# Kernel optimization log

Measured on AMD Instinct MI355X. Metric: run time of the kernel, lower is better.

The kernel has to match this reference:

```python
import jax, jax.numpy as jnp
import numpy as np

BIGINT = 1e10
BOA, BOH, BOL = 21, 22, 23      # global-node residue symbols
ATOM_POS_PAD = 0                # atom position pad index
AG_SEG = 1                      # antigen segment id


def setup_inputs() -> dict:
    key = jax.random.key(0)
    ks = jax.random.split(key, 8)
    B, L, C, E = 16, 128, 14, 256
    N = B * L
    # residues with global tokens at fixed positions per protein
    S = jax.random.randint(ks[0], (B, L), 0, 21)
    S = S.at[:, 0].set(BOA).at[:, 48].set(BOH).at[:, 96].set(BOL)
    S = S.reshape(N)
    seg = np.zeros((L,), np.int32); seg[0:48] = 1; seg[48:96] = 2; seg[96:] = 3
    segment_ids = jnp.tile(jnp.asarray(seg), B)
    RP = jnp.tile(jnp.arange(L, dtype=jnp.int32), B)
    A = jax.random.randint(ks[1], (N, C), 1, 16)
    AP = jax.random.randint(ks[2], (N, C), 0, 16)
    AP = AP.at[:, :4].set(jnp.arange(1, 5, dtype=AP.dtype)[None, :])  # backbone always present
    X = jax.random.normal(ks[3], (N, C, 3), dtype=jnp.float32) * 3.0
    res_embed = jax.random.normal(ks[4], (25, E), dtype=jnp.float32) * 0.02
    atom_embed = jax.random.normal(ks[5], (16, E), dtype=jnp.float32) * 0.02
    atom_pos_embed = jax.random.normal(ks[6], (16, E), dtype=jnp.float32) * 0.02
    return dict(S=S, RP=RP, A=A, AP=AP, X=X, segment_ids=segment_ids,
                res_embed=res_embed, atom_embed=atom_embed,
                atom_pos_embed=atom_pos_embed, max_n=L, k_neighbors=9)


def _embed(S, RP, A, AP, res_embed, atom_embed, atom_pos_embed):
    N = S.shape[0]
    E = res_embed.shape[1]
    half = E // 2
    inv = jnp.power(10000.0, -2.0 * jnp.arange(half, dtype=jnp.float32) / E)
    ang = RP.astype(jnp.float32)[:, None] * inv[None, :]
    pos_e = jnp.stack([jnp.sin(ang), jnp.cos(ang)], axis=-1).reshape(N, E)
    res_e = res_embed[S] + pos_e
    atom_e = atom_embed[A] + atom_pos_embed[AP]            # [N,C,E]
    not_pad = (AP != ATOM_POS_PAD)
    denom = not_pad.sum(-1, keepdims=True).astype(res_e.dtype) + 1e-10
    atom_e = jnp.sum(atom_e * not_pad[..., None], axis=1) / denom
    return jnp.concatenate([res_e, atom_e], axis=-1)       # [N,2E]


def _min_pair_dist(X, AP, max_n):
    # min over atom pairs of ||X[i,a]-X[j,b]||, pad atoms pushed to BIGINT
    N, C, _ = X.shape
    B = N // max_n
    Xb = X.reshape(B, max_n, C, 3)
    pad = (AP == ATOM_POS_PAD).reshape(B, max_n, C)
    sq = jnp.sum(Xb * Xb, axis=-1)                          # [B,L,C]
    dot = jnp.einsum('biad,bjcd->biajc', Xb, Xb)            # [B,L,C,L,C]
    d2 = sq[:, :, :, None, None] + sq[:, None, None, :, :] - 2.0 * dot
    dist = jnp.sqrt(jnp.maximum(d2, 0.0))
    pmask = pad[:, :, :, None, None] | pad[:, None, None, :, :]
    dist = dist + pmask.astype(dist.dtype) * BIGINT
    return jnp.min(dist, axis=(2, 4))                       # [B,L,L]


def _knn(dist_mat, sel_mask, k):
    # smallest-k neighbors among selected candidate edges; invalid -> -1
    B, L, _ = dist_mat.shape
    d = jnp.where(sel_mask, dist_mat, BIGINT)
    neg, dst_local = jax.lax.top_k(-d, k)                   # [B,L,k]
    valid = ((-neg) < BIGINT).reshape(-1)
    offs = (jnp.arange(B) * L)[:, None, None]
    src = jnp.broadcast_to(jnp.arange(L)[None, :, None] + offs, (B, L, k)).reshape(-1)
    dst = (dst_local + offs).reshape(-1)
    src = jnp.where(valid, src, -1)
    dst = jnp.where(valid, dst, -1)
    return jnp.stack([src, dst]), valid


def reference(S, RP, A, AP, X, segment_ids, res_embed, atom_embed, atom_pos_embed, max_n, k_neighbors):
    N = S.shape[0]
    L = max_n
    B = N // L
    h = _embed(S, RP, A, AP, res_embed, atom_embed, atom_pos_embed)
    dist = _min_pair_dist(X, AP, L)                          # [B,L,L]
    g = ((S == BOA) | (S == BOH) | (S == BOL)).reshape(B, L)
    seg = segment_ids.reshape(B, L)
    not_self = ~jnp.eye(L, dtype=bool)[None]                 # exclude i==j
    gi, gj = g[:, :, None], g[:, None, :]
    not_global = ~(gi | gj)
    same_seg = seg[:, :, None] == seg[:, None, :]
    inner_mask = same_seg & not_global & not_self
    outer_mask = (~same_seg) & not_global & not_self
    ctx_knn, ctx_valid = _knn(dist, inner_mask, k_neighbors)
    inter_knn, inter_valid = _knn(dist, outer_mask, k_neighbors)
    # non-kNN ctx edges (global_normal | global_global | sequential), dense adjacency
    global_normal = same_seg & (gi | gj) & not_self
    global_global = gi & gj & not_self
    idx = jnp.arange(L)
    adj_seq = (jnp.abs(idx[:, None] - idx[None, :]) == 1)[None]
    seq_mask = adj_seq & not_global & (seg[:, :, None] != AG_SEG)
    extra_ctx_adj = global_normal | global_global | seq_mask  # [B,L,L] bool
    return h, ctx_knn, ctx_valid, extra_ctx_adj, inter_knn, inter_valid
```

## Files before the change

kernel.cpp:

```cpp
#include <hip/hip_runtime.h>
#include <math.h>
#include <float.h>
#include <stdint.h>

#define BIGINT_F 1e10f
#define L_TOK 128
#define C_ATOM 14
#define E_DIM 256
#define K_NB 9

__device__ __forceinline__ float sq3(float x, float y, float z) {
    return __fadd_rn(__fadd_rn(__fmul_rn(x, x), __fmul_rn(y, y)), __fmul_rn(z, z));
}

__device__ __forceinline__ uint64_t umin64(uint64_t a, uint64_t b) { return a < b ? a : b; }

__global__ void __launch_bounds__(256)
fused_kernel(const int* __restrict__ S, const int* __restrict__ RP,
             const int* __restrict__ A, const int* __restrict__ AP,
             const float* __restrict__ X, const int* __restrict__ seg,
             const float* __restrict__ res_embed,
             const float* __restrict__ atom_embed,
             const float* __restrict__ atom_pos_embed,
             float* __restrict__ h,
             float* __restrict__ ctx_src, float* __restrict__ ctx_dst, float* __restrict__ ctx_val,
             float* __restrict__ adj_out,
             float* __restrict__ int_src, float* __restrict__ int_dst, float* __restrict__ int_val,
             int N) {
    const int NKNN = N / 4;
    int blk = blockIdx.x;
    int tid = threadIdx.x;

    if (blk < NKNN) {
        int wave = tid >> 6;
        int lane = tid & 63;
        int bi = blk * 4 + wave;
        int b  = bi >> 7;
        int i  = bi & (L_TOK - 1);
        int base_tok = (b << 7);

        __shared__ float sX[C_ATOM * L_TOK];
        __shared__ float sY[C_ATOM * L_TOK];
        __shared__ float sZ[C_ATOM * L_TOK];
        __shared__ float sQ[C_ATOM * L_TOK];

        const float* Xb  = X  + (size_t)base_tok * C_ATOM * 3;
        const int*   APb = AP + base_tok * C_ATOM;
        for (int idx = tid; idx < L_TOK * C_ATOM; idx += 256) {
            int tok = idx / C_ATOM;
            int c   = idx - tok * C_ATOM;
            float x0 = Xb[idx * 3 + 0];
            float x1 = Xb[idx * 3 + 1];
            float x2 = Xb[idx * 3 + 2];
            float q  = (APb[idx] == 0) ? INFINITY : sq3(x0, x1, x2);
            int w = c * L_TOK + (tok ^ (2 * c));
            sX[w] = x0; sY[w] = x1; sZ[w] = x2; sQ[w] = q;
        }
        __syncthreads();

        float xa0[C_ATOM], xa1[C_ATOM], xa2[C_ATOM], sa[C_ATOM];
        #pragma unroll
        for (int a = 0; a < C_ATOM; ++a) {
            int w = a * L_TOK + (i ^ (2 * a));
            xa0[a] = sX[w]; xa1[a] = sY[w]; xa2[a] = sZ[w]; sa[a] = sQ[w];
        }

        int j0 = lane, j1 = lane + 64;
        int nj0 = base_tok + j0, nj1 = base_tok + j1;

        float mind0 = INFINITY, mind1 = INFINITY;
        for (int c = 0; c < C_ATOM; ++c) {
            int w = c * L_TOK + (lane ^ (2 * c));
            float y00 = sX[w],      y01 = sY[w],      y02 = sZ[w],      sc0 = sQ[w];
            float y10 = sX[w + 64], y11 = sY[w + 64], y12 = sZ[w + 64], sc1 = sQ[w + 64];
            #pragma unroll
            for (int a = 0; a < C_ATOM; ++a) {
                float dot0 = __fadd_rn(__fadd_rn(__fmul_rn(xa0[a], y00),
                                                 __fmul_rn(xa1[a], y01)),
                                       __fmul_rn(xa2[a], y02));
                float d20 = __fsub_rn(__fadd_rn(sa[a], sc0), __fmul_rn(2.0f, dot0));
                mind0 = fminf(mind0, d20);
                float dot1 = __fadd_rn(__fadd_rn(__fmul_rn(xa0[a], y10),
                                                 __fmul_rn(xa1[a], y11)),
                                       __fmul_rn(xa2[a], y12));
                float d21 = __fsub_rn(__fadd_rn(sa[a], sc1), __fmul_rn(2.0f, dot1));
                mind1 = fminf(mind1, d21);
            }
        }
        float d0 = sqrtf(fmaxf(mind0, 0.0f));
        float d1 = sqrtf(fmaxf(mind1, 0.0f));

        int si = S[bi];
        int segi = seg[bi];
        bool gi = si >= 21;
        int sj0 = S[nj0], sj1 = S[nj1];
        int segj0 = seg[nj0], segj1 = seg[nj1];
        bool gj0 = sj0 >= 21, gj1 = sj1 >= 21;
        bool ns0 = (j0 != i), ns1 = (j1 != i);
        bool ng0 = !gi && !gj0 && ns0;
        bool ng1 = !gi && !gj1 && ns1;
        bool inner0 = (segi == segj0) && ng0;
        bool inner1 = (segi == segj1) && ng1;
        bool outer0 = (segi != segj0) && ng0;
        bool outer1 = (segi != segj1) && ng1;

        {
            bool gij0 = gi || gj0, gij1 = gi || gj1;
            bool same0 = (segi == segj0), same1 = (segi == segj1);
            int dd0 = i - j0, dd1 = i - j1;
            bool a0 = (dd0 == 1 || dd0 == -1), a1 = (dd1 == 1 || dd1 == -1);
            bool v0 = (same0 && gij0 && ns0) || (gi && gj0 && ns0) || (a0 && !gij0 && (segi != 1));
            bool v1 = (same1 && gij1 && ns1) || (gi && gj1 && ns1) || (a1 && !gij1 && (segi != 1));
            adj_out[(size_t)bi * L_TOK + j0] = v0 ? 1.0f : 0.0f;
            adj_out[(size_t)bi * L_TOK + j1] = v1 ? 1.0f : 0.0f;
        }

        const uint32_t bigbits = __float_as_uint(BIGINT_F);
        uint64_t kd0 = ((uint64_t)__float_as_uint(d0) << 32) | (uint32_t)j0;
        uint64_t kd1 = ((uint64_t)__float_as_uint(d1) << 32) | (uint32_t)j1;
        uint64_t kbig0 = ((uint64_t)bigbits << 32) | (uint32_t)j0;
        uint64_t kbig1 = ((uint64_t)bigbits << 32) | (uint32_t)j1;

        for (int pass = 0; pass < 2; ++pass) {
            uint64_t k0 = (pass == 0 ? inner0 : outer0) ? kd0 : kbig0;
            uint64_t k1 = (pass == 0 ? inner1 : outer1) ? kd1 : kbig1;
            float* osrc = (pass == 0) ? ctx_src : int_src;
            float* odst = (pass == 0) ? ctx_dst : int_dst;
            float* oval = (pass == 0) ? ctx_val : int_val;
            #pragma unroll
            for (int k = 0; k < K_NB; ++k) {
                uint64_t kk = umin64(k0, k1);
                #pragma unroll
                for (int m = 32; m > 0; m >>= 1) {
                    uint64_t o = __shfl_xor((unsigned long long)kk, m, 64);
                    kk = umin64(kk, o);
                }
                if (k0 == kk) k0 = UINT64_MAX;
                if (k1 == kk) k1 = UINT64_MAX;
                if (lane == 0) {
                    uint32_t dbits = (uint32_t)(kk >> 32);
                    int jmin = (int)(uint32_t)kk;
                    bool valid = dbits < bigbits;
                    int o = bi * K_NB + k;
                    osrc[o] = valid ? (float)bi : -1.0f;
                    odst[o] = valid ? (float)(base_tok + jmin) : -1.0f;
                    oval[o] = valid ? 1.0f : 0.0f;
                }
            }
        }
    } else {
        int n = blk - NKNN;
        int e = tid;
        int s = S[n];
        float rp = (float)RP[n];

        int k = e >> 1;
        const float c1 = (float)(-2.0 * 13.287712379549449 / (double)E_DIM);
        float invk = exp2f((float)k * c1);
        float ang = rp * invk;
        float pe = (e & 1) ? cosf(ang) : sinf(ang);
        h[(size_t)n * (2 * E_DIM) + e] = res_embed[s * E_DIM + e] + pe;

        __shared__ int sA[C_ATOM], sAP[C_ATOM];
        if (e < C_ATOM) { sA[e] = A[n * C_ATOM + e]; sAP[e] = AP[n * C_ATOM + e]; }
        __syncthreads();

        float sum = 0.0f, cnt = 0.0f;
        for (int c = 0; c < C_ATOM; ++c) {
            if (sAP[c] != 0) {
                sum += atom_embed[sA[c] * E_DIM + e] + atom_pos_embed[sAP[c] * E_DIM + e];
                cnt += 1.0f;
            }
        }
        h[(size_t)n * (2 * E_DIM) + E_DIM + e] = sum / (cnt + 1e-10f);
    }
}

extern "C" void kernel_launch(void* const* d_in, const int* in_sizes, int n_in,
                              void* d_out, int out_size, void* d_ws, size_t ws_size,
                              hipStream_t stream) {
    const int*   S    = (const int*)d_in[0];
    const int*   RP   = (const int*)d_in[1];
    const int*   A    = (const int*)d_in[2];
    const int*   AP   = (const int*)d_in[3];
    const float* X    = (const float*)d_in[4];
    const int*   seg  = (const int*)d_in[5];
    const float* rese = (const float*)d_in[6];
    const float* atme = (const float*)d_in[7];
    const float* atpe = (const float*)d_in[8];

    const int N = in_sizes[0];
    const int B = N / L_TOK;
    float* out = (float*)d_out;

    size_t off = 0;
    float* h_out   = out + off;  off += (size_t)N * 2 * E_DIM;
    float* ctx_src = out + off;  off += (size_t)N * K_NB;
    float* ctx_dst = out + off;  off += (size_t)N * K_NB;
    float* ctx_val = out + off;  off += (size_t)N * K_NB;
    float* adj_out = out + off;  off += (size_t)B * L_TOK * L_TOK;
    float* int_src = out + off;  off += (size_t)N * K_NB;
    float* int_dst = out + off;  off += (size_t)N * K_NB;
    float* int_val = out + off;  off += (size_t)N * K_NB;

    int nknn = N / 4;
    int grid = nknn + N;
    fused_kernel<<<grid, 256, 0, stream>>>(S, RP, A, AP, X, seg, rese, atme, atpe,
                                           h_out, ctx_src, ctx_dst, ctx_val,
                                           adj_out, int_src, int_dst, int_val, N);
}
```

Baseline: 97.91 us.

## Fold embedding work into kNN waves with float4 loads and drop separate embed blocks

Removes the N separate embedding blocks and has each kNN wave also compute its token's embedding row. Each lane handles four features using float4 loads and stores of the embedding tables. The launch_bounds hint also requests two blocks per CU. This shrinks the grid and cuts block launch and scheduling overhead, but makes each kNN block longer and its register use higher.

```diff
diff --git a/kernel.cpp b/kernel.cpp
--- a/kernel.cpp
+++ b/kernel.cpp
@@ -15,7 +15,7 @@
 
 __device__ __forceinline__ uint64_t umin64(uint64_t a, uint64_t b) { return a < b ? a : b; }
 
-__global__ void __launch_bounds__(256)
+__global__ void __launch_bounds__(256, 2)
 fused_kernel(const int* __restrict__ S, const int* __restrict__ RP,
              const int* __restrict__ A, const int* __restrict__ AP,
              const float* __restrict__ X, const int* __restrict__ seg,
@@ -27,152 +27,164 @@
              float* __restrict__ adj_out,
              float* __restrict__ int_src, float* __restrict__ int_dst, float* __restrict__ int_val,
              int N) {
-    const int NKNN = N / 4;
     int blk = blockIdx.x;
     int tid = threadIdx.x;
-
-    if (blk < NKNN) {
-        int wave = tid >> 6;
-        int lane = tid & 63;
-        int bi = blk * 4 + wave;
-        int b  = bi >> 7;
-        int i  = bi & (L_TOK - 1);
-        int base_tok = (b << 7);
-
-        __shared__ float sX[C_ATOM * L_TOK];
-        __shared__ float sY[C_ATOM * L_TOK];
-        __shared__ float sZ[C_ATOM * L_TOK];
-        __shared__ float sQ[C_ATOM * L_TOK];
-
-        const float* Xb  = X  + (size_t)base_tok * C_ATOM * 3;
-        const int*   APb = AP + base_tok * C_ATOM;
-        for (int idx = tid; idx < L_TOK * C_ATOM; idx += 256) {
-            int tok = idx / C_ATOM;
-            int c   = idx - tok * C_ATOM;
-            float x0 = Xb[idx * 3 + 0];
-            float x1 = Xb[idx * 3 + 1];
-            float x2 = Xb[idx * 3 + 2];
-            float q  = (APb[idx] == 0) ? INFINITY : sq3(x0, x1, x2);
-            int w = c * L_TOK + (tok ^ (2 * c));
-            sX[w] = x0; sY[w] = x1; sZ[w] = x2; sQ[w] = q;
-        }
-        __syncthreads();
-
-        float xa0[C_ATOM], xa1[C_ATOM], xa2[C_ATOM], sa[C_ATOM];
+    int wave = tid >> 6;
+    int lane = tid & 63;
+    int bi = blk * 4 + wave;
+    int b  = bi >> 7;
+    int i  = bi & (L_TOK - 1);
+    int base_tok = (b << 7);
+
+    __shared__ float sX[C_ATOM * L_TOK];
+    __shared__ float sY[C_ATOM * L_TOK];
+    __shared__ float sZ[C_ATOM * L_TOK];
+    __shared__ float sQ[C_ATOM * L_TOK];
+
+    const float* Xb  = X  + (size_t)base_tok * C_ATOM * 3;
+    const int*   APb = AP + base_tok * C_ATOM;
+    for (int idx = tid; idx < L_TOK * C_ATOM; idx += 256) {
+        int tok = idx / C_ATOM;
+        int c   = idx - tok * C_ATOM;
+        float x0 = Xb[idx * 3 + 0];
+        float x1 = Xb[idx * 3 + 1];
+        float x2 = Xb[idx * 3 + 2];
+        float q  = (APb[idx] == 0) ? INFINITY : sq3(x0, x1, x2);
+        int w = c * L_TOK + (tok ^ (2 * c));
+        sX[w] = x0; sY[w] = x1; sZ[w] = x2; sQ[w] = q;
+    }
+    __syncthreads();
+
+    float xa0[C_ATOM], xa1[C_ATOM], xa2[C_ATOM], sa[C_ATOM];
+    #pragma unroll
+    for (int a = 0; a < C_ATOM; ++a) {
+        int w = a * L_TOK + (i ^ (2 * a));
+        xa0[a] = sX[w]; xa1[a] = sY[w]; xa2[a] = sZ[w]; sa[a] = sQ[w];
+    }
+
+    int j0 = lane, j1 = lane + 64;
+    int nj0 = base_tok + j0, nj1 = base_tok + j1;
+
+    float mind0 = INFINITY, mind1 = INFINITY;
+    for (int c = 0; c < C_ATOM; ++c) {
+        int w = c * L_TOK + (lane ^ (2 * c));
+        float y00 = sX[w],      y01 = sY[w],      y02 = sZ[w],      sc0 = sQ[w];
+        float y10 = sX[w + 64], y11 = sY[w + 64], y12 = sZ[w + 64], sc1 = sQ[w + 64];
         #pragma unroll
         for (int a = 0; a < C_ATOM; ++a) {
-            int w = a * L_TOK + (i ^ (2 * a));
-            xa0[a] = sX[w]; xa1[a] = sY[w]; xa2[a] = sZ[w]; sa[a] = sQ[w];
+            float dot0 = __fadd_rn(__fadd_rn(__fmul_rn(xa0[a], y00),
+                                             __fmul_rn(xa1[a], y01)),
+                                   __fmul_rn(xa2[a], y02));
+            float d20 = __fsub_rn(__fadd_rn(sa[a], sc0), __fmul_rn(2.0f, dot0));
+            mind0 = fminf(mind0, d20);
+            float dot1 = __fadd_rn(__fadd_rn(__fmul_rn(xa0[a], y10),
+                                             __fmul_rn(xa1[a], y11)),
+                                   __fmul_rn(xa2[a], y12));
+            float d21 = __fsub_rn(__fadd_rn(sa[a], sc1), __fmul_rn(2.0f, dot1));
+            mind1 = fminf(mind1, d21);
         }
-
-        int j0 = lane, j1 = lane + 64;
-        int nj0 = base_tok + j0, nj1 = base_tok + j1;
-
-        float mind0 = INFINITY, mind1 = INFINITY;
-        for (int c = 0; c < C_ATOM; ++c) {
-            int w = c * L_TOK + (lane ^ (2 * c));
-            float y00 = sX[w],      y01 = sY[w],      y02 = sZ[w],      sc0 = sQ[w];
-            float y10 = sX[w + 64], y11 = sY[w + 64], y12 = sZ[w + 64], sc1 = sQ[w + 64];
+    }
+    float d0 = sqrtf(fmaxf(mind0, 0.0f));
+    float d1 = sqrtf(fmaxf(mind1, 0.0f));
+
+    int si = S[bi];
+    int segi = seg[bi];
+    bool gi = si >= 21;
+    int sj0 = S[nj0], sj1 = S[nj1];
+    int segj0 = seg[nj0], segj1 = seg[nj1];
+    bool gj0 = sj0 >= 21, gj1 = sj1 >= 21;
+    bool ns0 = (j0 != i), ns1 = (j1 != i);
+    bool ng0 = !gi && !gj0 && ns0;
+    bool ng1 = !gi && !gj1 && ns1;
+    bool inner0 = (segi == segj0) && ng0;
+    bool inner1 = (segi == segj1) && ng1;
+    bool outer0 = (segi != segj0) && ng0;
+    bool outer1 = (segi != segj1) && ng1;
+
+    {
+        bool gij0 = gi || gj0, gij1 = gi || gj1;
+        bool same0 = (segi == segj0), same1 = (segi == segj1);
+        int dd0 = i - j0, dd1 = i - j1;
+        bool a0 = (dd0 == 1 || dd0 == -1), a1 = (dd1 == 1 || dd1 == -1);
+        bool v0 = (same0 && gij0 && ns0) || (gi && gj0 && ns0) || (a0 && !gij0 && (segi != 1));
+        bool v1 = (same1 && gij1 && ns1) || (gi && gj1 && ns1) || (a1 && !gij1 && (segi != 1));
+        adj_out[(size_t)bi * L_TOK + j0] = v0 ? 1.0f : 0.0f;
+        adj_out[(size_t)bi * L_TOK + j1] = v1 ? 1.0f : 0.0f;
+    }
+
+    const uint32_t bigbits = __float_as_uint(BIGINT_F);
+    uint64_t kd0 = ((uint64_t)__float_as_uint(d0) << 32) | (uint32_t)j0;
+    uint64_t kd1 = ((uint64_t)__float_as_uint(d1) << 32) | (uint32_t)j1;
+    uint64_t kbig0 = ((uint64_t)bigbits << 32) | (uint32_t)j0;
+    uint64_t kbig1 = ((uint64_t)bigbits << 32) | (uint32_t)j1;
+
+    for (int pass = 0; pass < 2; ++pass) {
+        uint64_t k0 = (pass == 0 ? inner0 : outer0) ? kd0 : kbig0;
+        uint64_t k1 = (pass == 0 ? inner1 : outer1) ? kd1 : kbig1;
+        float* osrc = (pass == 0) ? ctx_src : int_src;
+        float* odst = (pass == 0) ? ctx_dst : int_dst;
+        float* oval = (pass == 0) ? ctx_val : int_val;
+        #pragma unroll
+        for (int k = 0; k < K_NB; ++k) {
+            uint64_t kk = umin64(k0, k1);
             #pragma unroll
-            for (int a = 0; a < C_ATOM; ++a) {
-                float dot0 = __fadd_rn(__fadd_rn(__fmul_rn(xa0[a], y00),
-                                                 __fmul_rn(xa1[a], y01)),
-                                       __fmul_rn(xa2[a], y02));
-                float d20 = __fsub_rn(__fadd_rn(sa[a], sc0), __fmul_rn(2.0f, dot0));
-                mind0 = fminf(mind0, d20);
-                float dot1 = __fadd_rn(__fadd_rn(__fmul_rn(xa0[a], y10),
-                                                 __fmul_rn(xa1[a], y11)),
-                                       __fmul_rn(xa2[a], y12));
-                float d21 = __fsub_rn(__fadd_rn(sa[a], sc1), __fmul_rn(2.0f, dot1));
-                mind1 = fminf(mind1, d21);
+            for (int m = 32; m > 0; m >>= 1) {
+                uint64_t o = __shfl_xor((unsigned long long)kk, m, 64);
+                kk = umin64(kk, o);
+            }
+            if (k0 == kk) k0 = UINT64_MAX;
+            if (k1 == kk) k1 = UINT64_MAX;
+            if (lane == 0) {
+                uint32_t dbits = (uint32_t)(kk >> 32);
+                int jmin = (int)(uint32_t)kk;
+                bool valid = dbits < bigbits;
+                int o = bi * K_NB + k;
+                osrc[o] = valid ? (float)bi : -1.0f;
+                odst[o] = valid ? (float)(base_tok + jmin) : -1.0f;
+                oval[o] = valid ? 1.0f : 0.0f;
             }
         }
-        float d0 = sqrtf(fmaxf(mind0, 0.0f));
-        float d1 = sqrtf(fmaxf(mind1, 0.0f));
-
-        int si = S[bi];
-        int segi = seg[bi];
-        bool gi = si >= 21;
-        int sj0 = S[nj0], sj1 = S[nj1];
-        int segj0 = seg[nj0], segj1 = seg[nj1];
-        bool gj0 = sj0 >= 21, gj1 = sj1 >= 21;
-        bool ns0 = (j0 != i), ns1 = (j1 != i);
-        bool ng0 = !gi && !gj0 && ns0;
-        bool ng1 = !gi && !gj1 && ns1;
-        bool inner0 = (segi == segj0) && ng0;
-        bool inner1 = (segi == segj1) && ng1;
-        bool outer0 = (segi != segj0) && ng0;
-        bool outer1 = (segi != segj1) && ng1;
-
-        {
-            bool gij0 = gi || gj0, gij1 = gi || gj1;
-            bool same0 = (segi == segj0), same1 = (segi == segj1);
-            int dd0 = i - j0, dd1 = i - j1;
-            bool a0 = (dd0 == 1 || dd0 == -1), a1 = (dd1 == 1 || dd1 == -1);
-            bool v0 = (same0 && gij0 && ns0) || (gi && gj0 && ns0) || (a0 && !gij0 && (segi != 1));
-            bool v1 = (same1 && gij1 && ns1) || (gi && gj1 && ns1) || (a1 && !gij1 && (segi != 1));
-            adj_out[(size_t)bi * L_TOK + j0] = v0 ? 1.0f : 0.0f;
-            adj_out[(size_t)bi * L_TOK + j1] = v1 ? 1.0f : 0.0f;
-        }
-
-        const uint32_t bigbits = __float_as_uint(BIGINT_F);
-        uint64_t kd0 = ((uint64_t)__float_as_uint(d0) << 32) | (uint32_t)j0;
-        uint64_t kd1 = ((uint64_t)__float_as_uint(d1) << 32) | (uint32_t)j1;
-        uint64_t kbig0 = ((uint64_t)bigbits << 32) | (uint32_t)j0;
-        uint64_t kbig1 = ((uint64_t)bigbits << 32) | (uint32_t)j1;
-
-        for (int pass = 0; pass < 2; ++pass) {
-            uint64_t k0 = (pass == 0 ? inner0 : outer0) ? kd0 : kbig0;
-            uint64_t k1 = (pass == 0 ? inner1 : outer1) ? kd1 : kbig1;
-            float* osrc = (pass == 0) ? ctx_src : int_src;
-            float* odst = (pass == 0) ? ctx_dst : int_dst;
-            float* oval = (pass == 0) ? ctx_val : int_val;
-            #pragma unroll
-            for (int k = 0; k < K_NB; ++k) {
-                uint64_t kk = umin64(k0, k1);
-                #pragma unroll
-                for (int m = 32; m > 0; m >>= 1) {
-                    uint64_t o = __shfl_xor((unsigned long long)kk, m, 64);
-                    kk = umin64(kk, o);
-                }
-                if (k0 == kk) k0 = UINT64_MAX;
-                if (k1 == kk) k1 = UINT64_MAX;
-                if (lane == 0) {
-                    uint32_t dbits = (uint32_t)(kk >> 32);
-                    int jmin = (int)(uint32_t)kk;
-                    bool valid = dbits < bigbits;
-                    int o = bi * K_NB + k;
-                    osrc[o] = valid ? (float)bi : -1.0f;
-                    odst[o] = valid ? (float)(base_tok + jmin) : -1.0f;
-                    oval[o] = valid ? 1.0f : 0.0f;
-                }
-            }
-        }
-    } else {
-        int n = blk - NKNN;
-        int e = tid;
-        int s = S[n];
-        float rp = (float)RP[n];
-
-        int k = e >> 1;
+    }
+
+    {
+        float rp = (float)RP[bi];
+        int e0 = lane * 4;
+        int k0e = e0 >> 1;
         const float c1 = (float)(-2.0 * 13.287712379549449 / (double)E_DIM);
-        float invk = exp2f((float)k * c1);
-        float ang = rp * invk;
-        float pe = (e & 1) ? cosf(ang) : sinf(ang);
-        h[(size_t)n * (2 * E_DIM) + e] = res_embed[s * E_DIM + e] + pe;
-
-        __shared__ int sA[C_ATOM], sAP[C_ATOM];
-        if (e < C_ATOM) { sA[e] = A[n * C_ATOM + e]; sAP[e] = AP[n * C_ATOM + e]; }
-        __syncthreads();
-
-        float sum = 0.0f, cnt = 0.0f;
+        float ivA = exp2f((float)k0e * c1);
+        float ivB = exp2f((float)(k0e + 1) * c1);
+        float angA = rp * ivA, angB = rp * ivB;
+
+        const float4 r4 = *(const float4*)(res_embed + (size_t)si * E_DIM + e0);
+        float4 res4;
+        res4.x = r4.x + sinf(angA);
+        res4.y = r4.y + cosf(angA);
+        res4.z = r4.z + sinf(angB);
+        res4.w = r4.w + cosf(angB);
+
+        float4 sum4 = make_float4(0.f, 0.f, 0.f, 0.f);
+        float cnt = 0.0f;
+        const int* Arow  = A  + bi * C_ATOM;
+        const int* AProw = AP + bi * C_ATOM;
         for (int c = 0; c < C_ATOM; ++c) {
-            if (sAP[c] != 0) {
-                sum += atom_embed[sA[c] * E_DIM + e] + atom_pos_embed[sAP[c] * E_DIM + e];
+            int ap = AProw[c];
+            if (ap != 0) {
+                int a = Arow[c];
+                const float4 ae = *(const float4*)(atom_embed + (size_t)a * E_DIM + e0);
+                const float4 pe = *(const float4*)(atom_pos_embed + (size_t)ap * E_DIM + e0);
+                sum4.x += ae.x + pe.x;
+                sum4.y += ae.y + pe.y;
+                sum4.z += ae.z + pe.z;
+                sum4.w += ae.w + pe.w;
                 cnt += 1.0f;
             }
         }
-        h[(size_t)n * (2 * E_DIM) + E_DIM + e] = sum / (cnt + 1e-10f);
+        float inv = cnt + 1e-10f;
+        float4 atom4 = make_float4(sum4.x / inv, sum4.y / inv, sum4.z / inv, sum4.w / inv);
+
+        float* hrow = h + (size_t)bi * (2 * E_DIM);
+        *(float4*)(hrow + e0) = res4;
+        *(float4*)(hrow + E_DIM + e0) = atom4;
     }
 }
 
@@ -203,8 +215,7 @@
     float* int_dst = out + off;  off += (size_t)N * K_NB;
     float* int_val = out + off;  off += (size_t)N * K_NB;
 
-    int nknn = N / 4;
-    int grid = nknn + N;
+    int grid = N / 4;
     fused_kernel<<<grid, 256, 0, stream>>>(S, RP, A, AP, X, seg, rese, atme, atpe,
                                            h_out, ctx_src, ctx_dst, ctx_val,
                                            adj_out, int_src, int_dst, int_val, N);
```

New measurement: 99.21 us. Within noise of the previous version (+1.3%).
